# Optimization experiments

Measured on AMD Instinct MI355X. Metric: run time of the kernel, lower is better.

Reference implementation:

```python
import jax, jax.numpy as jnp
import numpy as np

B, S, E = 8, 2048, 1024


def setup_inputs() -> dict:
    key = jax.random.key(0)
    ks = jax.random.split(key, 8)
    scale = 1.0 / np.sqrt(E)
    x = jax.random.normal(ks[0], (B, S, E), dtype=jnp.float32)
    Wq = jax.random.uniform(ks[1], (E, E), jnp.float32, -scale, scale)
    bq = jax.random.uniform(ks[2], (E,), jnp.float32, -scale, scale)
    Wk = jax.random.uniform(ks[3], (E, E), jnp.float32, -scale, scale)
    bk = jax.random.uniform(ks[4], (E,), jnp.float32, -scale, scale)
    Wv = jax.random.uniform(ks[5], (E, E), jnp.float32, -scale, scale)
    bv = jax.random.uniform(ks[6], (E,), jnp.float32, -scale, scale)
    # key-padding mask: True = fill position (broadcasts over query dim)
    mask = jax.random.randint(ks[7], (B, 1, S), 0, 2) > 0
    return {"x": x, "Wq": Wq, "bq": bq, "Wk": Wk, "bk": bk, "Wv": Wv, "bv": bv, "mask": mask}


def reference(x, Wq, bq, Wk, bk, Wv, bv, mask):
    # torch Linear: y = x @ W.T + b
    q = jnp.einsum('bse,fe->bsf', x, Wq) + bq
    k = jnp.einsum('bse,fe->bsf', x, Wk) + bk
    v = jnp.einsum('bse,fe->bsf', x, Wv) + bv
    inv_sqrt_d = 1.0 / jnp.sqrt(jnp.asarray(E, x.dtype))
    A = jnp.einsum('bqe,bke->bqk', q, k) * inv_sqrt_d  # (B, S, S)
    # non-standard masked_fill: fills with 1e-9 (NOT -inf), pre-softmax
    A = jnp.where(mask, jnp.asarray(1e-9, A.dtype), A)
    A = jax.nn.softmax(A, axis=-1)
    out = jnp.einsum('bqk,bke->bqe', A, v)
    # dropout is identity at inference
    return out
```

## Files before the change

kernel.cpp:

```cpp
#include <hip/hip_runtime.h>
#include <hip/hip_bf16.h>

#define B_ 8
#define S_ 2048
#define E_ 1024

using f32x4 = __attribute__((ext_vector_type(4))) float;
using s16x8 = __attribute__((ext_vector_type(8))) short;
using u16x8 = __attribute__((ext_vector_type(8))) unsigned short;

typedef __attribute__((address_space(1))) unsigned int glb_u32;
typedef __attribute__((address_space(3))) unsigned int lds_u32;

#define FENCE() __builtin_amdgcn_sched_barrier(0)

static __device__ __forceinline__ unsigned short f2bf(float f) {
    union { float f; unsigned int u; } v; v.f = f;
    unsigned int u = v.u;
    u += 0x7FFFu + ((u >> 16) & 1u);
    return (unsigned short)(u >> 16);
}
static __device__ __forceinline__ float bf2f(unsigned short h) {
    union { unsigned int u; float f; } v; v.u = ((unsigned int)h) << 16;
    return v.f;
}

__global__ __launch_bounds__(256) void mask_canon_kernel(
    const unsigned char* __restrict__ src, unsigned char* __restrict__ dst, int n)
{
    __shared__ int flags;
    if (threadIdx.x == 0) flags = 0;
    __syncthreads();
    int f = 0;
    for (int j = threadIdx.x; j < n; j += 256) {
        unsigned char b = src[j];
        if (b) {
            int p = j & 3;
            if (p == 1) f |= 1;
            if (p >= 2) f |= 2;
        }
    }
    if (f) atomicOr(&flags, f);
    __syncthreads();
    const int fl = flags;
    for (int i = threadIdx.x; i < n; i += 256) {
        unsigned char v;
        if (fl & 1)      v = (unsigned char)(src[i] != 0);
        else if (fl & 2) v = (unsigned char)(((const float*)(const void*)src)[i] != 0.0f);
        else             v = (unsigned char)(((const int*)(const void*)src)[i] != 0);
        dst[i] = v;
    }
}

__global__ __launch_bounds__(256) void cvt_bf16_kernel(
    const float* __restrict__ src, unsigned short* __restrict__ dst, int n8)
{
    const int stride = gridDim.x * 256;
    for (int i = blockIdx.x * 256 + threadIdx.x; i < n8; i += stride) {
        float4 a = *(const float4*)(src + (size_t)i * 8);
        float4 b = *(const float4*)(src + (size_t)i * 8 + 4);
        u16x8 o;
        o[0]=f2bf(a.x); o[1]=f2bf(a.y); o[2]=f2bf(a.z); o[3]=f2bf(a.w);
        o[4]=f2bf(b.x); o[5]=f2bf(b.y); o[6]=f2bf(b.z); o[7]=f2bf(b.w);
        *(u16x8*)(dst + (size_t)i * 8) = o;
    }
}

template<int EPI>
__global__ __launch_bounds__(512, 2) void gemm256(
    const unsigned short* __restrict__ A, const unsigned short* __restrict__ B,
    void* __restrict__ Cout,
    long long sAz, long long sBz, long long sCz,
    int lda, int ldb, int ldc, int K,
    const unsigned char* __restrict__ mask, int maskStride, float scale,
    const float* __restrict__ bias)
{
    __shared__ unsigned short lds[65536];
    const int tid = threadIdx.x;
    const int lane = tid & 63, w = tid >> 6;
    const int wr = w >> 2, wc = w & 3;
    const int fr = lane & 15, ch = lane >> 4;

    const int gx = gridDim.x, gy = gridDim.y;
    const int nwg = gx * gy * gridDim.z;
    int bid = blockIdx.x + gx * (blockIdx.y + gy * blockIdx.z);
    bid = (bid & 7) * (nwg >> 3) + (bid >> 3);
    const int bx = bid % gx; int tmp = bid / gx;
    const int by = tmp % gy; const int bz = tmp / gy;

    const unsigned short* Ab = A + (size_t)bz * sAz;
    const unsigned short* Bb = B + (size_t)bz * sBz;
    const int m0 = by * 256, n0 = bx * 256;

    const int rdlane = fr * 32 + ((ch * 8) ^ ((fr & 8) ? 16 : 0));
    const int local = (lane * 16) ^ (lane & 32);
    const int rloc = local >> 6;
    const int cloc = (local >> 4) & 3;

    f32x4 acc[8][4] = {};
    const int NT = K >> 6;

    auto STAGE = [&](const unsigned short* __restrict__ src, int ld, int base,
                     int ts, int half, int matoff, unsigned bo) {
        const int k0 = ts * 64;
        const int rowb = half * 128 + w * 16;
        #pragma unroll
        for (int kk = 0; kk < 2; ++kk) {
            const unsigned short* g = src + (size_t)(base + rowb + rloc) * ld
                                          + (k0 + kk * 32 + cloc * 8);
            __builtin_amdgcn_global_load_lds((const glb_u32*)g,
                (lds_u32*)&lds[bo + matoff + kk * 8192 + rowb * 32], 16, 0, 0);
        }
    };

    STAGE(Ab, lda, m0, 0, 0, 0, 0);      STAGE(Ab, lda, m0, 0, 1, 0, 0);
    STAGE(Bb, ldb, n0, 0, 0, 16384, 0);  STAGE(Bb, ldb, n0, 0, 1, 16384, 0);
    STAGE(Ab, lda, m0, 1, 0, 0, 32768);  STAGE(Ab, lda, m0, 1, 1, 0, 32768);
    STAGE(Bb, ldb, n0, 1, 0, 16384, 32768);
    asm volatile("s_waitcnt vmcnt(6)" ::: "memory");
    __builtin_amdgcn_s_barrier();

    for (int t = 0; t < NT; ++t) {
        const unsigned bo = (unsigned)(t & 1) * 32768u;
        const unsigned nbo = bo ^ 32768u;
        const int tp1 = (t + 1 < NT) ? t + 1 : NT - 1;
        const int tp2 = (t + 2 < NT) ? t + 2 : NT - 1;

        s16x8 af[8][2], bfv[4][2];
        #pragma unroll
        for (int i = 0; i < 4; ++i)
            #pragma unroll
            for (int kk = 0; kk < 2; ++kk)
                af[i][kk] = *(const s16x8*)&lds[bo + kk * 8192 + (wr * 128 + i * 16) * 32 + rdlane];
        #pragma unroll
        for (int j = 0; j < 2; ++j)
            #pragma unroll
            for (int kk = 0; kk < 2; ++kk)
                bfv[j][kk] = *(const s16x8*)&lds[bo + 16384 + kk * 8192 + (wc * 64 + j * 16) * 32 + rdlane];
        #pragma unroll
        for (int i = 4; i < 8; ++i)
            #pragma unroll
            for (int kk = 0; kk < 2; ++kk)
                af[i][kk] = *(const s16x8*)&lds[bo + kk * 8192 + (wr * 128 + i * 16) * 32 + rdlane];
        #pragma unroll
        for (int j = 2; j < 4; ++j)
            #pragma unroll
            for (int kk = 0; kk < 2; ++kk)
                bfv[j][kk] = *(const s16x8*)&lds[bo + 16384 + kk * 8192 + (wc * 64 + j * 16) * 32 + rdlane];
        STAGE(Bb, ldb, n0, tp1, 1, 16384, nbo);
        __builtin_amdgcn_s_barrier();
        FENCE();
        __builtin_amdgcn_s_setprio(1);
        #pragma unroll
        for (int i = 0; i < 4; ++i)
            #pragma unroll
            for (int j = 0; j < 2; ++j)
                #pragma unroll
                for (int kk = 0; kk < 2; ++kk)
                    acc[i][j] = __builtin_amdgcn_mfma_f32_16x16x32_bf16(af[i][kk], bfv[j][kk], acc[i][j], 0, 0, 0);
        __builtin_amdgcn_s_setprio(0);
        FENCE();
        asm volatile("s_waitcnt lgkmcnt(0)" ::: "memory");
        FENCE();
        __builtin_amdgcn_s_barrier();
        STAGE(Ab, lda, m0, tp2, 0, 0, bo);
        __builtin_amdgcn_s_barrier();
        FENCE();
        __builtin_amdgcn_s_setprio(1);
        #pragma unroll
        for (int i = 0; i < 4; ++i)
            #pragma unroll
            for (int j = 0; j < 2; ++j)
                #pragma unroll
                for (int kk = 0; kk < 2; ++kk)
                    acc[i][2 + j] = __builtin_amdgcn_mfma_f32_16x16x32_bf16(af[i][kk], bfv[2 + j][kk], acc[i][2 + j], 0, 0, 0);
        __builtin_amdgcn_s_setprio(0);
        FENCE();
        __builtin_amdgcn_s_barrier();
        STAGE(Ab, lda, m0, tp2, 1, 0, bo);
        __builtin_amdgcn_s_barrier();
        FENCE();
        __builtin_amdgcn_s_setprio(1);
        #pragma unroll
        for (int i = 0; i < 4; ++i)
            #pragma unroll
            for (int j = 0; j < 2; ++j)
                #pragma unroll
                for (int kk = 0; kk < 2; ++kk)
                    acc[4 + i][j] = __builtin_amdgcn_mfma_f32_16x16x32_bf16(af[4 + i][kk], bfv[j][kk], acc[4 + i][j], 0, 0, 0);
        __builtin_amdgcn_s_setprio(0);
        FENCE();
        __builtin_amdgcn_s_barrier();
        STAGE(Bb, ldb, n0, tp2, 0, 16384, bo);
        __builtin_amdgcn_s_barrier();
        FENCE();
        __builtin_amdgcn_s_setprio(1);
        #pragma unroll
        for (int i = 0; i < 4; ++i)
            #pragma unroll
            for (int j = 0; j < 2; ++j)
                #pragma unroll
                for (int kk = 0; kk < 2; ++kk)
                    acc[4 + i][2 + j] = __builtin_amdgcn_mfma_f32_16x16x32_bf16(af[4 + i][kk], bfv[2 + j][kk], acc[4 + i][2 + j], 0, 0, 0);
        __builtin_amdgcn_s_setprio(0);
        FENCE();
        asm volatile("s_waitcnt vmcnt(6)" ::: "memory");
        FENCE();
        __builtin_amdgcn_s_barrier();
    }

    if constexpr (EPI == 1) {
        float* Cb = (float*)Cout + (size_t)bz * sCz;
        #pragma unroll
        for (int j = 0; j < 4; ++j) {
            const int ncol = n0 + wc * 64 + j * 16 + fr;
            #pragma unroll
            for (int i = 0; i < 8; ++i)
                #pragma unroll
                for (int r = 0; r < 4; ++r) {
                    const int mrow = m0 + wr * 128 + i * 16 + ch * 4 + r;
                    Cb[(size_t)mrow * ldc + ncol] = acc[i][j][r];
                }
        }
    } else {
        unsigned short* Cb = (unsigned short*)Cout + (size_t)bz * sCz;
        const unsigned char* mb = (EPI == 0) ? mask + (size_t)bz * maskStride : nullptr;
        #pragma unroll
        for (int j = 0; j < 4; ++j) {
            const int ncol = n0 + wc * 64 + j * 16 + fr;
            bool msk = false; float bn = 0.f;
            if constexpr (EPI == 0) msk = mb[ncol] != 0;
            if constexpr (EPI == 2) bn = bias[ncol];
            #pragma unroll
            for (int i = 0; i < 8; ++i) {
                #pragma unroll
                for (int r = 0; r < 4; ++r) {
                    const int mrow = m0 + wr * 128 + i * 16 + ch * 4 + r;
                    float val;
                    if constexpr (EPI == 0)      val = msk ? 1e-9f : acc[i][j][r] * scale;
                    else if constexpr (EPI == 2) val = acc[i][j][r] + bn;
                    else                         val = acc[i][j][r] + bias[mrow];
                    Cb[(size_t)mrow * ldc + ncol] = f2bf(val);
                }
            }
        }
    }
}

__global__ __launch_bounds__(256) void softmax_kernel(unsigned short* __restrict__ P)
{
    const int row = blockIdx.x;
    const int tid = threadIdx.x;
    unsigned short* prow = P + (size_t)row * S_;
    u16x8 v = *(const u16x8*)&prow[tid * 8];
    float f[8];
    #pragma unroll
    for (int j = 0; j < 8; ++j) f[j] = bf2f(v[j]);
    float m = f[0];
    #pragma unroll
    for (int j = 1; j < 8; ++j) m = fmaxf(m, f[j]);
    #pragma unroll
    for (int o = 1; o < 64; o <<= 1) m = fmaxf(m, __shfl_xor(m, o, 64));
    __shared__ float smax[4], ssum[4];
    const int w = tid >> 6, lane = tid & 63;
    if (lane == 0) smax[w] = m;
    __syncthreads();
    m = fmaxf(fmaxf(smax[0], smax[1]), fmaxf(smax[2], smax[3]));
    float e[8], s = 0.f;
    #pragma unroll
    for (int j = 0; j < 8; ++j) { e[j] = expf(f[j] - m); s += e[j]; }
    #pragma unroll
    for (int o = 1; o < 64; o <<= 1) s += __shfl_xor(s, o, 64);
    if (lane == 0) ssum[w] = s;
    __syncthreads();
    s = ssum[0] + ssum[1] + ssum[2] + ssum[3];
    const float inv = 1.0f / s;
    u16x8 o8;
    #pragma unroll
    for (int j = 0; j < 8; ++j) o8[j] = f2bf(e[j] * inv);
    *(u16x8*)&prow[tid * 8] = o8;
}

extern "C" void kernel_launch(void* const* d_in, const int* in_sizes, int n_in,
                              void* d_out, int out_size, void* d_ws, size_t ws_size,
                              hipStream_t stream)
{
    const float* x  = (const float*)d_in[0];
    const float* Wq = (const float*)d_in[1];
    const float* bq = (const float*)d_in[2];
    const float* Wk = (const float*)d_in[3];
    const float* bk = (const float*)d_in[4];
    const float* Wv = (const float*)d_in[5];
    const float* bv = (const float*)d_in[6];
    const unsigned char* mraw = (const unsigned char*)d_in[7];

    const int BS = B_ * S_;
    unsigned short* Qb = (unsigned short*)d_ws;
    unsigned short* Kb = Qb + (size_t)BS * E_;
    unsigned short* VT = Kb + (size_t)BS * E_;
    unsigned short* Sc = VT + (size_t)BS * E_;
    unsigned short* xb = Sc;
    unsigned short* Wqb = Sc + (size_t)BS * E_;
    unsigned short* Wkb = Wqb + (size_t)E_ * E_;
    unsigned short* Wvb = Wkb + (size_t)E_ * E_;
    unsigned char* mcanon = (unsigned char*)(Sc + (size_t)B_ * S_ * S_);

    mask_canon_kernel<<<1, 256, 0, stream>>>(mraw, mcanon, BS);

    cvt_bf16_kernel<<<2048, 256, 0, stream>>>(x, xb, BS * E_ / 8);
    cvt_bf16_kernel<<<512, 256, 0, stream>>>(Wq, Wqb, E_ * E_ / 8);
    cvt_bf16_kernel<<<512, 256, 0, stream>>>(Wk, Wkb, E_ * E_ / 8);
    cvt_bf16_kernel<<<512, 256, 0, stream>>>(Wv, Wvb, E_ * E_ / 8);

    gemm256<2><<<dim3(E_ / 256, BS / 256), 512, 0, stream>>>(
        xb, Wqb, (void*)Qb, 0, 0, 0, E_, E_, E_, E_, nullptr, 0, 1.0f, bq);
    gemm256<2><<<dim3(E_ / 256, BS / 256), 512, 0, stream>>>(
        xb, Wkb, (void*)Kb, 0, 0, 0, E_, E_, E_, E_, nullptr, 0, 1.0f, bk);
    gemm256<3><<<dim3(BS / 256, E_ / 256), 512, 0, stream>>>(
        Wvb, xb, (void*)VT, 0, 0, 0, E_, E_, BS, E_, nullptr, 0, 1.0f, bv);

    gemm256<0><<<dim3(S_ / 256, S_ / 256, B_), 512, 0, stream>>>(
        Qb, Kb, (void*)Sc,
        (long long)S_ * E_, (long long)S_ * E_, (long long)S_ * S_,
        E_, E_, S_, E_, mcanon, S_, 0.03125f, nullptr);

    softmax_kernel<<<dim3(BS), 256, 0, stream>>>(Sc);

    gemm256<1><<<dim3(E_ / 256, S_ / 256, B_), 512, 0, stream>>>(
        Sc, VT, d_out,
        (long long)S_ * S_, (long long)S_, (long long)S_ * E_,
        S_, BS, E_, S_, nullptr, 0, 1.0f, nullptr);
}
```

Measured before the change: 364.6 us.

## Cut GEMM main-loop barriers and merge fp32-to-bf16 conversions into one launch

```diff
diff --git a/kernel.cpp b/kernel.cpp
--- a/kernel.cpp
+++ b/kernel.cpp
@@ -52,17 +52,27 @@
     }
 }
 
-__global__ __launch_bounds__(256) void cvt_bf16_kernel(
-    const float* __restrict__ src, unsigned short* __restrict__ dst, int n8)
-{
+__global__ __launch_bounds__(256) void cvt_all_kernel(
+    const float* __restrict__ x,  unsigned short* __restrict__ xb,
+    const float* __restrict__ w0, unsigned short* __restrict__ d0,
+    const float* __restrict__ w1, unsigned short* __restrict__ d1,
+    const float* __restrict__ w2, unsigned short* __restrict__ d2,
+    int nx8, int nw8)
+{
+    const int total = nx8 + 3 * nw8;
     const int stride = gridDim.x * 256;
-    for (int i = blockIdx.x * 256 + threadIdx.x; i < n8; i += stride) {
-        float4 a = *(const float4*)(src + (size_t)i * 8);
-        float4 b = *(const float4*)(src + (size_t)i * 8 + 4);
+    for (int i = blockIdx.x * 256 + threadIdx.x; i < total; i += stride) {
+        const float* s; unsigned short* d; int k;
+        if (i < nx8)                { s = x;  d = xb; k = i; }
+        else if (i < nx8 + nw8)     { s = w0; d = d0; k = i - nx8; }
+        else if (i < nx8 + 2 * nw8) { s = w1; d = d1; k = i - nx8 - nw8; }
+        else                        { s = w2; d = d2; k = i - nx8 - 2 * nw8; }
+        float4 a = *(const float4*)(s + (size_t)k * 8);
+        float4 b = *(const float4*)(s + (size_t)k * 8 + 4);
         u16x8 o;
         o[0]=f2bf(a.x); o[1]=f2bf(a.y); o[2]=f2bf(a.z); o[3]=f2bf(a.w);
         o[4]=f2bf(b.x); o[5]=f2bf(b.y); o[6]=f2bf(b.z); o[7]=f2bf(b.w);
-        *(u16x8*)(dst + (size_t)i * 8) = o;
+        *(u16x8*)(d + (size_t)k * 8) = o;
     }
 }
 
@@ -137,6 +147,7 @@
             #pragma unroll
             for (int kk = 0; kk < 2; ++kk)
                 bfv[j][kk] = *(const s16x8*)&lds[bo + 16384 + kk * 8192 + (wc * 64 + j * 16) * 32 + rdlane];
+        FENCE();
         #pragma unroll
         for (int i = 4; i < 8; ++i)
             #pragma unroll
@@ -148,7 +159,8 @@
             for (int kk = 0; kk < 2; ++kk)
                 bfv[j][kk] = *(const s16x8*)&lds[bo + 16384 + kk * 8192 + (wc * 64 + j * 16) * 32 + rdlane];
         STAGE(Bb, ldb, n0, tp1, 1, 16384, nbo);
-        __builtin_amdgcn_s_barrier();
+        FENCE();
+        asm volatile("s_waitcnt lgkmcnt(12)" ::: "memory");
         FENCE();
         __builtin_amdgcn_s_setprio(1);
         #pragma unroll
@@ -162,10 +174,6 @@
         FENCE();
         asm volatile("s_waitcnt lgkmcnt(0)" ::: "memory");
         FENCE();
-        __builtin_amdgcn_s_barrier();
-        STAGE(Ab, lda, m0, tp2, 0, 0, bo);
-        __builtin_amdgcn_s_barrier();
-        FENCE();
         __builtin_amdgcn_s_setprio(1);
         #pragma unroll
         for (int i = 0; i < 4; ++i)
@@ -177,8 +185,10 @@
         __builtin_amdgcn_s_setprio(0);
         FENCE();
         __builtin_amdgcn_s_barrier();
+        FENCE();
+        STAGE(Bb, ldb, n0, tp2, 0, 16384, bo);
+        STAGE(Ab, lda, m0, tp2, 0, 0, bo);
         STAGE(Ab, lda, m0, tp2, 1, 0, bo);
-        __builtin_amdgcn_s_barrier();
         FENCE();
         __builtin_amdgcn_s_setprio(1);
         #pragma unroll
@@ -188,13 +198,6 @@
                 #pragma unroll
                 for (int kk = 0; kk < 2; ++kk)
                     acc[4 + i][j] = __builtin_amdgcn_mfma_f32_16x16x32_bf16(af[4 + i][kk], bfv[j][kk], acc[4 + i][j], 0, 0, 0);
-        __builtin_amdgcn_s_setprio(0);
-        FENCE();
-        __builtin_amdgcn_s_barrier();
-        STAGE(Bb, ldb, n0, tp2, 0, 16384, bo);
-        __builtin_amdgcn_s_barrier();
-        FENCE();
-        __builtin_amdgcn_s_setprio(1);
         #pragma unroll
         for (int i = 0; i < 4; ++i)
             #pragma unroll
@@ -307,10 +310,8 @@
 
     mask_canon_kernel<<<1, 256, 0, stream>>>(mraw, mcanon, BS);
 
-    cvt_bf16_kernel<<<2048, 256, 0, stream>>>(x, xb, BS * E_ / 8);
-    cvt_bf16_kernel<<<512, 256, 0, stream>>>(Wq, Wqb, E_ * E_ / 8);
-    cvt_bf16_kernel<<<512, 256, 0, stream>>>(Wk, Wkb, E_ * E_ / 8);
-    cvt_bf16_kernel<<<512, 256, 0, stream>>>(Wv, Wvb, E_ * E_ / 8);
+    cvt_all_kernel<<<2048, 256, 0, stream>>>(
+        x, xb, Wq, Wqb, Wk, Wkb, Wv, Wvb, BS * E_ / 8, E_ * E_ / 8);
 
     gemm256<2><<<dim3(E_ / 256, BS / 256), 512, 0, stream>>>(
         xb, Wqb, (void*)Qb, 0, 0, 0, E_, E_, E_, E_, nullptr, 0, 1.0f, bq);
```

Result: faster. 347.7 us (-4.6%).
